# Optimization experiments

Hardware: AMD Instinct MI355X
Metric: run time of the kernel (lower is better)

Reference implementation:

```python
import jax, jax.numpy as jnp
import numpy as np

B, S, IN_DIM = 16, 1024, 64
D, H, FF, L, OUT = 512, 8, 2048, 6, 256
HD = D // H
EPS = 1e-5


def _ln(x, g, b):
    m = jnp.mean(x, axis=-1, keepdims=True)
    v = jnp.var(x, axis=-1, keepdims=True)
    return (x - m) * jax.lax.rsqrt(v + EPS) * g + b


def setup_inputs() -> dict:
    key = jax.random.key(0)
    ks = jax.random.split(key, 24)
    def rn(k, shape, scale=0.02):
        return jax.random.normal(k, shape, dtype=jnp.float32) * scale
    return {
        "x": jax.random.normal(ks[0], (B, S, IN_DIM), dtype=jnp.float32),
        "in_w": rn(ks[1], (IN_DIM, D)), "in_b": jnp.zeros((D,), jnp.float32),
        "in_ln_g": jnp.ones((D,), jnp.float32), "in_ln_b": jnp.zeros((D,), jnp.float32),
        "pos": rn(ks[2], (S, D)),
        "qkv_w": rn(ks[3], (L, D, 3 * D)), "qkv_b": jnp.zeros((L, 3 * D), jnp.float32),
        "ao_w": rn(ks[4], (L, D, D)), "ao_b": jnp.zeros((L, D), jnp.float32),
        "ff_w1": rn(ks[5], (L, D, FF)), "ff_b1": jnp.zeros((L, FF), jnp.float32),
        "ff_w2": rn(ks[6], (L, FF, D)), "ff_b2": jnp.zeros((L, D), jnp.float32),
        "ln1_g": jnp.ones((L, D), jnp.float32), "ln1_b": jnp.zeros((L, D), jnp.float32),
        "ln2_g": jnp.ones((L, D), jnp.float32), "ln2_b": jnp.zeros((L, D), jnp.float32),
        "o_w1": rn(ks[7], (D, D // 2)), "o_b1": jnp.zeros((D // 2,), jnp.float32),
        "o_ln_g": jnp.ones((D // 2,), jnp.float32), "o_ln_b": jnp.zeros((D // 2,), jnp.float32),
        "o_w2": rn(ks[8], (D // 2, OUT)), "o_b2": jnp.zeros((OUT,), jnp.float32),
    }


def reference(x, in_w, in_b, in_ln_g, in_ln_b, pos,
              qkv_w, qkv_b, ao_w, ao_b, ff_w1, ff_b1, ff_w2, ff_b2,
              ln1_g, ln1_b, ln2_g, ln2_b,
              o_w1, o_b1, o_ln_g, o_ln_b, o_w2, o_b2):
    h = x @ in_w + in_b                      # [B,S,D]
    h = _ln(h, in_ln_g, in_ln_b)
    h = h + pos[None, :, :]
    scale = 1.0 / jnp.sqrt(jnp.float32(HD))
    for l in range(L):
        qkv = h @ qkv_w[l] + qkv_b[l]        # [B,S,3D]
        q, k, v = jnp.split(qkv, 3, axis=-1)
        q = q.reshape(B, S, H, HD)
        k = k.reshape(B, S, H, HD)
        v = v.reshape(B, S, H, HD)
        scores = jnp.einsum('bqhd,bkhd->bhqk', q, k) * scale
        attn = jax.nn.softmax(scores, axis=-1)
        ctx = jnp.einsum('bhqk,bkhd->bqhd', attn, v).reshape(B, S, D)
        attn_out = ctx @ ao_w[l] + ao_b[l]
        h = _ln(h + attn_out, ln1_g[l], ln1_b[l])
        ff = jax.nn.gelu(h @ ff_w1[l] + ff_b1[l], approximate=False) @ ff_w2[l] + ff_b2[l]
        h = _ln(h + ff, ln2_g[l], ln2_b[l])
    pooled = jnp.mean(h, axis=1)             # [B,D]
    z = jax.nn.gelu(pooled @ o_w1 + o_b1, approximate=False)
    z = _ln(z, o_ln_g, o_ln_b)
    return z @ o_w2 + o_b2                   # [B,OUT]
```

## Files before the change

### kernel.cpp

```cpp
#include <hip/hip_runtime.h>
#include <hip/hip_bf16.h>

#define B_ 16
#define S_ 1024
#define IN_ 64
#define D_ 512
#define H_ 8
#define HD_ 64
#define FF_ 2048
#define L_ 6
#define OUT_ 256
#define BS_ (B_*S_)

typedef __attribute__((ext_vector_type(8))) short s16x8;
typedef __attribute__((ext_vector_type(4))) short s16x4;
typedef __attribute__((ext_vector_type(4))) float f32x4;

#define AS1(p) ((const __attribute__((address_space(1))) void*)(p))
#define AS3(p) ((__attribute__((address_space(3))) void*)(p))

__device__ __forceinline__ ushort f2bf(float x) {
  __hip_bfloat16 h = __float2bfloat16(x);
  return *reinterpret_cast<ushort*>(&h);
}
__device__ __forceinline__ float bf2f(ushort u) {
  unsigned v = ((unsigned)u) << 16;
  union { unsigned u; float f; } c; c.u = v; return c.f;
}
__device__ __forceinline__ float gelu_exact(float x) {
  return 0.5f * x * (1.0f + erff(x * 0.70710678118654752f));
}

template<int BN, int WM, int WN, int MODE>
__global__ __launch_bounds__(256)
void gemm_bt(const ushort* __restrict__ A, int lda,
             const ushort* __restrict__ Bt, int ldb,
             const float* __restrict__ bias,
             ushort* __restrict__ C, int ldc,
             int K)
{
  constexpr int BM = 128;
  constexpr int BK = 64;
  constexpr int FM = BM / (WM * 16);
  constexpr int FN = BN / (WN * 16);
  __shared__ ushort As[BM * BK];
  __shared__ ushort Bs[BN * BK];

  const int tid = threadIdx.x;
  const int lane = tid & 63;
  const int wave = tid >> 6;
  const int wr = wave / WN;
  const int wc = wave % WN;
  const int lrow = lane & 15;
  const int lk = (lane >> 4) * 8;

  const int gx = gridDim.x;
  const int nwg = gx * gridDim.y;
  const int flat = blockIdx.y * gx + blockIdx.x;
  const int T = (flat & 7) * (nwg >> 3) + (flat >> 3);
  const int m0 = (T / gx) * BM;
  const int n0 = (T % gx) * BN;

  f32x4 acc[FM][FN];
#pragma unroll
  for (int m = 0; m < FM; ++m)
#pragma unroll
    for (int n = 0; n < FN; ++n)
      acc[m][n] = (f32x4){0.f, 0.f, 0.f, 0.f};

  for (int k0 = 0; k0 < K; k0 += BK) {
    __syncthreads();
#pragma unroll
    for (int rr = 0; rr < BM / 32; ++rr) {
      int c = rr * 256 + tid;
      int row = c >> 3, cg = c & 7;
      __builtin_amdgcn_global_load_lds(
          AS1(A + (size_t)(m0 + row) * lda + k0 + cg * 8),
          AS3(As + (size_t)(rr * 256 + wave * 64) * 8), 16, 0, 0);
    }
#pragma unroll
    for (int rr = 0; rr < BN / 32; ++rr) {
      int c = rr * 256 + tid;
      int row = c >> 3, cg = c & 7;
      __builtin_amdgcn_global_load_lds(
          AS1(Bt + (size_t)(n0 + row) * ldb + k0 + cg * 8),
          AS3(Bs + (size_t)(rr * 256 + wave * 64) * 8), 16, 0, 0);
    }
    __syncthreads();
#pragma unroll
    for (int kk = 0; kk < 2; ++kk) {
      s16x8 a[FM], b[FN];
#pragma unroll
      for (int m = 0; m < FM; ++m)
        a[m] = *(const s16x8*)&As[(wr * FM * 16 + m * 16 + lrow) * BK + kk * 32 + lk];
#pragma unroll
      for (int n = 0; n < FN; ++n)
        b[n] = *(const s16x8*)&Bs[(wc * FN * 16 + n * 16 + lrow) * BK + kk * 32 + lk];
#pragma unroll
      for (int m = 0; m < FM; ++m)
#pragma unroll
        for (int n = 0; n < FN; ++n)
          acc[m][n] = __builtin_amdgcn_mfma_f32_16x16x32_bf16(a[m], b[n], acc[m][n], 0, 0, 0);
    }
  }

  const int rb = m0 + wr * FM * 16 + (lane >> 4) * 4;
  const int cb = n0 + wc * FN * 16 + lrow;
#pragma unroll
  for (int n = 0; n < FN; ++n) {
    int col = cb + n * 16;
    float bv = bias ? bias[col] : 0.0f;
#pragma unroll
    for (int m = 0; m < FM; ++m) {
      int row = rb + m * 16;
#pragma unroll
      for (int r = 0; r < 4; ++r) {
        float v = acc[m][n][r] + bv;
        size_t idx = (size_t)(row + r) * ldc + col;
        if (MODE == 1) C[idx] = f2bf(v);
        else           C[idx] = f2bf(gelu_exact(v));
      }
    }
  }
}

__global__ __launch_bounds__(512)
void flash_kernel(const ushort* __restrict__ qkv, const ushort* __restrict__ vt,
                  ushort* __restrict__ ctx)
{
  constexpr int KB = 128;
  const float KE = 0.125f * 1.44269504f;
  __shared__ ushort ks[KB][72];
  __shared__ ushort vs[HD_][KB + 8];
  const int tid = threadIdx.x;
  const int lane = tid & 63;
  const int wave = tid >> 6;
  const int lrow = lane & 15;
  const int g = lane >> 4;
  const int lk = g * 8;

  const int flat = blockIdx.y * 8 + blockIdx.x;
  const int T = (flat & 7) * 128 + (flat >> 3);
  const int bh = T >> 3;
  const int b = bh >> 3, h = bh & 7;
  const int q0 = (T & 7) * 128;

  s16x8 qf[2];
  {
    const ushort* qrow = qkv + ((size_t)(b * S_ + q0 + wave * 16 + lrow)) * (3 * D_) + h * HD_;
    s16x8 r0 = *(const s16x8*)(qrow + lk);
    s16x8 r1 = *(const s16x8*)(qrow + 32 + lk);
#pragma unroll
    for (int j = 0; j < 8; ++j) {
      qf[0][j] = (short)f2bf(bf2f((ushort)r0[j]) * KE);
      qf[1][j] = (short)f2bf(bf2f((ushort)r1[j]) * KE);
    }
  }
  float lsum = 0.f;
  f32x4 o[4] = {};

  for (int kt = 0; kt < S_ / KB; ++kt) {
    __syncthreads();
    for (int c = tid; c < KB * 8; c += 512) {
      int row = c >> 3, cg = c & 7;
      *(s16x8*)&ks[row][cg * 8] =
          *(const s16x8*)(qkv + ((size_t)(b * S_ + kt * KB + row)) * (3 * D_) + D_ + h * HD_ + cg * 8);
    }
    for (int c = tid; c < HD_ * 16; c += 512) {
      int row = c >> 4, cg = c & 15;
      *(s16x8*)&vs[row][cg * 8] =
          *(const s16x8*)(vt + ((size_t)(bh * HD_ + row)) * S_ + kt * KB + cg * 8);
    }
    __syncthreads();

#pragma unroll
    for (int tp = 0; tp < 4; ++tp) {
      f32x4 s0 = {}, s1 = {};
      {
        s16x8 k00 = *(const s16x8*)&ks[tp * 32 + lrow][lk];
        s16x8 k01 = *(const s16x8*)&ks[tp * 32 + lrow][32 + lk];
        s16x8 k10 = *(const s16x8*)&ks[tp * 32 + 16 + lrow][lk];
        s16x8 k11 = *(const s16x8*)&ks[tp * 32 + 16 + lrow][32 + lk];
        s0 = __builtin_amdgcn_mfma_f32_16x16x32_bf16(k00, qf[0], s0, 0, 0, 0);
        s0 = __builtin_amdgcn_mfma_f32_16x16x32_bf16(k01, qf[1], s0, 0, 0, 0);
        s1 = __builtin_amdgcn_mfma_f32_16x16x32_bf16(k10, qf[0], s1, 0, 0, 0);
        s1 = __builtin_amdgcn_mfma_f32_16x16x32_bf16(k11, qf[1], s1, 0, 0, 0);
      }
      union { s16x8 v; unsigned u[4]; } pa;
      {
        float p0 = exp2f(s0[0]), p1 = exp2f(s0[1]);
        float p2 = exp2f(s0[2]), p3 = exp2f(s0[3]);
        float p4 = exp2f(s1[0]), p5 = exp2f(s1[1]);
        float p6 = exp2f(s1[2]), p7 = exp2f(s1[3]);
        lsum += ((p0 + p1) + (p2 + p3)) + ((p4 + p5) + (p6 + p7));
        unsigned u0 = __float_as_uint(p0) + 0x8000u, u1 = __float_as_uint(p1) + 0x8000u;
        unsigned u2 = __float_as_uint(p2) + 0x8000u, u3 = __float_as_uint(p3) + 0x8000u;
        unsigned u4 = __float_as_uint(p4) + 0x8000u, u5 = __float_as_uint(p5) + 0x8000u;
        unsigned u6 = __float_as_uint(p6) + 0x8000u, u7 = __float_as_uint(p7) + 0x8000u;
        pa.u[0] = (u0 >> 16) | (u1 & 0xffff0000u);
        pa.u[1] = (u2 >> 16) | (u3 & 0xffff0000u);
        pa.u[2] = (u4 >> 16) | (u5 & 0xffff0000u);
        pa.u[3] = (u6 >> 16) | (u7 & 0xffff0000u);
      }
#pragma unroll
      for (int n2 = 0; n2 < 4; ++n2) {
        s16x8 vf = *(const s16x8*)&vs[n2 * 16 + lrow][tp * 32 + lk];
        o[n2] = __builtin_amdgcn_mfma_f32_16x16x32_bf16(vf, pa.v, o[n2], 0, 0, 0);
      }
    }
  }
  lsum += __shfl_xor(lsum, 16);
  lsum += __shfl_xor(lsum, 32);
  float inv = 1.0f / lsum;

  ushort* crow = ctx + ((size_t)(b * S_ + q0 + wave * 16 + lrow)) * D_ + h * HD_;
#pragma unroll
  for (int n2 = 0; n2 < 4; ++n2) {
    s16x4 w;
#pragma unroll
    for (int r = 0; r < 4; ++r) w[r] = (short)f2bf(o[n2][r] * inv);
    *(s16x4*)(crow + n2 * 16 + g * 4) = w;
  }
}

__global__ __launch_bounds__(256)
void ln512_kernel(const ushort* __restrict__ a, const ushort* __restrict__ res,
                  const float* __restrict__ g, const float* __restrict__ bt,
                  const float* __restrict__ pos,
                  ushort* __restrict__ hout)
{
  const int row = blockIdx.x;
  const int t = threadIdx.x;
  const size_t base = (size_t)row * D_;
  float x0 = bf2f(a[base + t]), x1 = bf2f(a[base + t + 256]);
  if (res) { x0 += bf2f(res[base + t]); x1 += bf2f(res[base + t + 256]); }
  float s = x0 + x1, q = x0 * x0 + x1 * x1;
#pragma unroll
  for (int m = 32; m > 0; m >>= 1) { s += __shfl_xor(s, m); q += __shfl_xor(q, m); }
  __shared__ float red[8];
  if ((t & 63) == 0) { red[(t >> 6) * 2] = s; red[(t >> 6) * 2 + 1] = q; }
  __syncthreads();
  s = red[0] + red[2] + red[4] + red[6];
  q = red[1] + red[3] + red[5] + red[7];
  float mean = s * (1.0f / D_);
  float var = q * (1.0f / D_) - mean * mean;
  float rs = rsqrtf(var + 1e-5f);
  float y0 = (x0 - mean) * rs * g[t] + bt[t];
  float y1 = (x1 - mean) * rs * g[t + 256] + bt[t + 256];
  if (pos) {
    int sp = row & (S_ - 1);
    y0 += pos[(size_t)sp * D_ + t];
    y1 += pos[(size_t)sp * D_ + t + 256];
  }
  hout[base + t] = f2bf(y0);
  hout[base + t + 256] = f2bf(y1);
}

__global__ __launch_bounds__(256)
void vtrans_kernel(const ushort* __restrict__ qkv, ushort* __restrict__ vt)
{
  __shared__ ushort tile[64][72];
  const int bh = blockIdx.x;
  const int b = bh >> 3, h = bh & 7;
  const int k0 = blockIdx.y * 64;
  const int t = threadIdx.x;
  for (int c = t; c < 512; c += 256) {
    int row = c >> 3, dg = c & 7;
    *(s16x8*)&tile[row][dg * 8] =
        *(const s16x8*)(qkv + (size_t)(b * S_ + k0 + row) * (3 * D_) + 2 * D_ + h * HD_ + dg * 8);
  }
  __syncthreads();
  int d = t >> 2, gg = t & 3;
#pragma unroll
  for (int w = 0; w < 2; ++w) {
    ushort out[8];
#pragma unroll
    for (int j = 0; j < 8; ++j) {
      int lkk = w * 32 + (j < 4 ? 4 * gg + j : 16 + 4 * gg + (j - 4));
      out[j] = tile[lkk][d];
    }
    *(s16x8*)&vt[((size_t)bh * HD_ + d) * S_ + k0 + w * 32 + gg * 8] = *(s16x8*)out;
  }
}

__global__ void wtrans_kernel(const float* __restrict__ W, ushort* __restrict__ Wt, int K, int N)
{
  __shared__ float tile[32][33];
  const float* Wl = W + (size_t)blockIdx.z * K * N;
  ushort* Wtl = Wt + (size_t)blockIdx.z * K * N;
  int n0 = blockIdx.x * 32, k0 = blockIdx.y * 32;
  int tx = threadIdx.x, ty = threadIdx.y;
#pragma unroll
  for (int r = 0; r < 4; ++r)
    tile[ty * 4 + r][tx] = Wl[(size_t)(k0 + ty * 4 + r) * N + n0 + tx];
  __syncthreads();
#pragma unroll
  for (int r = 0; r < 4; ++r)
    Wtl[(size_t)(n0 + ty * 4 + r) * K + k0 + tx] = f2bf(tile[tx][ty * 4 + r]);
}

__global__ void castx_kernel(const float* __restrict__ x, ushort* __restrict__ xb, int n)
{
  int i = blockIdx.x * blockDim.x + threadIdx.x;
  if (i < n) xb[i] = f2bf(x[i]);
}

__global__ __launch_bounds__(256)
void pool_partial_kernel(const ushort* __restrict__ h, float* __restrict__ pp)
{
  int b = blockIdx.x, ch = blockIdx.y;
  int t = threadIdx.x;
  float s0 = 0, s1 = 0;
  for (int r = 0; r < 128; ++r) {
    size_t base = ((size_t)b * S_ + ch * 128 + r) * D_;
    s0 += bf2f(h[base + t]);
    s1 += bf2f(h[base + t + 256]);
  }
  pp[(size_t)(b * 8 + ch) * D_ + t] = s0;
  pp[(size_t)(b * 8 + ch) * D_ + t + 256] = s1;
}

__global__ __launch_bounds__(256)
void head_kernel(const float* __restrict__ pp,
                 const float* __restrict__ w1, const float* __restrict__ b1,
                 const float* __restrict__ lg, const float* __restrict__ lb,
                 const float* __restrict__ w2, const float* __restrict__ b2,
                 float* __restrict__ out)
{
  __shared__ float pooled[D_];
  __shared__ float z[256];
  int b = blockIdx.x, t = threadIdx.x;
  for (int i = t; i < D_; i += 256) {
    float s = 0;
    for (int c = 0; c < 8; ++c) s += pp[(size_t)(b * 8 + c) * D_ + i];
    pooled[i] = s * (1.0f / S_);
  }
  __syncthreads();
  float acc = 0;
  for (int k = 0; k < D_; ++k) acc += pooled[k] * w1[(size_t)k * 256 + t];
  float zz = gelu_exact(acc + b1[t]);
  float s = zz, q = zz * zz;
#pragma unroll
  for (int m = 32; m > 0; m >>= 1) { s += __shfl_xor(s, m); q += __shfl_xor(q, m); }
  __shared__ float red[8];
  if ((t & 63) == 0) { red[(t >> 6) * 2] = s; red[(t >> 6) * 2 + 1] = q; }
  __syncthreads();
  s = red[0] + red[2] + red[4] + red[6];
  q = red[1] + red[3] + red[5] + red[7];
  float mean = s * (1.0f / 256), var = q * (1.0f / 256) - mean * mean;
  float rs = rsqrtf(var + 1e-5f);
  z[t] = (zz - mean) * rs * lg[t] + lb[t];
  __syncthreads();
  float o = 0;
  for (int k = 0; k < 256; ++k) o += z[k] * w2[(size_t)k * 256 + t];
  out[(size_t)b * 256 + t] = o + b2[t];
}

extern "C" void kernel_launch(void* const* d_in, const int* in_sizes, int n_in,
                              void* d_out, int out_size, void* d_ws, size_t ws_size,
                              hipStream_t stream)
{
  const float* x       = (const float*)d_in[0];
  const float* in_w    = (const float*)d_in[1];
  const float* in_b    = (const float*)d_in[2];
  const float* in_ln_g = (const float*)d_in[3];
  const float* in_ln_b = (const float*)d_in[4];
  const float* pos     = (const float*)d_in[5];
  const float* qkv_w   = (const float*)d_in[6];
  const float* qkv_b   = (const float*)d_in[7];
  const float* ao_w    = (const float*)d_in[8];
  const float* ao_b    = (const float*)d_in[9];
  const float* ff_w1   = (const float*)d_in[10];
  const float* ff_b1   = (const float*)d_in[11];
  const float* ff_w2   = (const float*)d_in[12];
  const float* ff_b2   = (const float*)d_in[13];
  const float* ln1_g   = (const float*)d_in[14];
  const float* ln1_b   = (const float*)d_in[15];
  const float* ln2_g   = (const float*)d_in[16];
  const float* ln2_b   = (const float*)d_in[17];
  const float* o_w1    = (const float*)d_in[18];
  const float* o_b1    = (const float*)d_in[19];
  const float* o_ln_g  = (const float*)d_in[20];
  const float* o_ln_b  = (const float*)d_in[21];
  const float* o_w2    = (const float*)d_in[22];
  const float* o_b2    = (const float*)d_in[23];

  char* wp = (char*)d_ws;
  auto alloc = [&](size_t bytes) {
    char* p = wp;
    wp += (bytes + 255) & ~(size_t)255;
    return p;
  };
  ushort* hb     = (ushort*)alloc((size_t)BS_ * D_ * 2);
  ushort* tmpb   = (ushort*)alloc((size_t)BS_ * D_ * 2);
  ushort* big    = (ushort*)alloc((size_t)BS_ * FF_ * 2);
  ushort* ctxb   = (ushort*)alloc((size_t)BS_ * D_ * 2);
  ushort* xb     = (ushort*)alloc((size_t)BS_ * IN_ * 2);
  ushort* vt     = (ushort*)alloc((size_t)B_ * H_ * HD_ * S_ * 2);
  float*  pp     = (float*) alloc((size_t)B_ * 8 * D_ * 4);
  ushort* in_wt  = (ushort*)alloc((size_t)D_ * IN_ * 2);
  ushort* qkv_wt = (ushort*)alloc((size_t)L_ * 3 * D_ * D_ * 2);
  ushort* ao_wt  = (ushort*)alloc((size_t)L_ * D_ * D_ * 2);
  ushort* ff1_wt = (ushort*)alloc((size_t)L_ * FF_ * D_ * 2);
  ushort* ff2_wt = (ushort*)alloc((size_t)L_ * D_ * FF_ * 2);
  (void)ws_size; (void)n_in; (void)in_sizes; (void)out_size;

  dim3 wb(32, 8);
  wtrans_kernel<<<dim3(D_ / 32, IN_ / 32, 1), wb, 0, stream>>>(in_w, in_wt, IN_, D_);
  wtrans_kernel<<<dim3(3 * D_ / 32, D_ / 32, L_), wb, 0, stream>>>(qkv_w, qkv_wt, D_, 3 * D_);
  wtrans_kernel<<<dim3(D_ / 32, D_ / 32, L_), wb, 0, stream>>>(ao_w, ao_wt, D_, D_);
  wtrans_kernel<<<dim3(FF_ / 32, D_ / 32, L_), wb, 0, stream>>>(ff_w1, ff1_wt, D_, FF_);
  wtrans_kernel<<<dim3(D_ / 32, FF_ / 32, L_), wb, 0, stream>>>(ff_w2, ff2_wt, FF_, D_);
  castx_kernel<<<BS_ * IN_ / 256, 256, 0, stream>>>(x, xb, BS_ * IN_);

  gemm_bt<128, 2, 2, 1><<<dim3(D_ / 128, BS_ / 128), 256, 0, stream>>>(
      xb, IN_, in_wt, IN_, in_b, tmpb, D_, IN_);
  ln512_kernel<<<BS_, 256, 0, stream>>>(tmpb, nullptr, in_ln_g, in_ln_b, pos, hb);

  for (int l = 0; l < L_; ++l) {
    gemm_bt<128, 2, 2, 1><<<dim3(3 * D_ / 128, BS_ / 128), 256, 0, stream>>>(
        hb, D_, qkv_wt + (size_t)l * 3 * D_ * D_, D_, qkv_b + (size_t)l * 3 * D_,
        big, 3 * D_, D_);
    vtrans_kernel<<<dim3(B_ * H_, S_ / 64), 256, 0, stream>>>(big, vt);
    flash_kernel<<<dim3(S_ / 128, B_ * H_), 512, 0, stream>>>(big, vt, ctxb);
    gemm_bt<128, 2, 2, 1><<<dim3(D_ / 128, BS_ / 128), 256, 0, stream>>>(
        ctxb, D_, ao_wt + (size_t)l * D_ * D_, D_, ao_b + (size_t)l * D_,
        tmpb, D_, D_);
    ln512_kernel<<<BS_, 256, 0, stream>>>(tmpb, hb, ln1_g + (size_t)l * D_,
                                          ln1_b + (size_t)l * D_, nullptr, hb);
    gemm_bt<128, 2, 2, 2><<<dim3(FF_ / 128, BS_ / 128), 256, 0, stream>>>(
        hb, D_, ff1_wt + (size_t)l * FF_ * D_, D_, ff_b1 + (size_t)l * FF_,
        big, FF_, D_);
    gemm_bt<128, 2, 2, 1><<<dim3(D_ / 128, BS_ / 128), 256, 0, stream>>>(
        big, FF_, ff2_wt + (size_t)l * D_ * FF_, FF_, ff_b2 + (size_t)l * D_,
        tmpb, D_, FF_);
    ln512_kernel<<<BS_, 256, 0, stream>>>(tmpb, hb, ln2_g + (size_t)l * D_,
                                          ln2_b + (size_t)l * D_, nullptr, hb);
  }
  pool_partial_kernel<<<dim3(B_, 8), 256, 0, stream>>>(hb, pp);
  head_kernel<<<B_, 256, 0, stream>>>(pp, o_w1, o_b1, o_ln_g, o_ln_b, o_w2, o_b2,
                                      (float*)d_out);
}
```

Before: 1.813 ms.

## Stage GEMM epilogue through LDS and fuse V transpose into QKV GEMM

The GEMM epilogue now writes results into a shared-memory tile that reuses the A/B staging buffers, then emits coalesced 16-byte global stores instead of scattered 2-byte stores. A new MODE 3 writes the V projection straight into the transposed per-head layout the flash kernel expects. The QKV GEMM is split into a Q/K launch and a V launch, which removes the separate vtrans kernel and its extra read and write of V. In exchange there is an extra launch, one more barrier per tile, and LDS bank traffic in the epilogue.

```diff
diff --git a/kernel.cpp b/kernel.cpp
--- a/kernel.cpp
+++ b/kernel.cpp
@@ -43,8 +43,11 @@
   constexpr int BK = 64;
   constexpr int FM = BM / (WM * 16);
   constexpr int FN = BN / (WN * 16);
-  __shared__ ushort As[BM * BK];
-  __shared__ ushort Bs[BN * BK];
+  constexpr int CP = 136;
+  __shared__ union {
+    struct { ushort a[BM * BK]; ushort b[BN * BK]; } s;
+    ushort c[BM * CP];
+  } u;
 
   const int tid = threadIdx.x;
   const int lane = tid & 63;
@@ -76,7 +79,7 @@
       int row = c >> 3, cg = c & 7;
       __builtin_amdgcn_global_load_lds(
           AS1(A + (size_t)(m0 + row) * lda + k0 + cg * 8),
-          AS3(As + (size_t)(rr * 256 + wave * 64) * 8), 16, 0, 0);
+          AS3(u.s.a + (size_t)(rr * 256 + wave * 64) * 8), 16, 0, 0);
     }
 #pragma unroll
     for (int rr = 0; rr < BN / 32; ++rr) {
@@ -84,7 +87,7 @@
       int row = c >> 3, cg = c & 7;
       __builtin_amdgcn_global_load_lds(
           AS1(Bt + (size_t)(n0 + row) * ldb + k0 + cg * 8),
-          AS3(Bs + (size_t)(rr * 256 + wave * 64) * 8), 16, 0, 0);
+          AS3(u.s.b + (size_t)(rr * 256 + wave * 64) * 8), 16, 0, 0);
     }
     __syncthreads();
 #pragma unroll
@@ -92,10 +95,10 @@
       s16x8 a[FM], b[FN];
 #pragma unroll
       for (int m = 0; m < FM; ++m)
-        a[m] = *(const s16x8*)&As[(wr * FM * 16 + m * 16 + lrow) * BK + kk * 32 + lk];
+        a[m] = *(const s16x8*)&u.s.a[(wr * FM * 16 + m * 16 + lrow) * BK + kk * 32 + lk];
 #pragma unroll
       for (int n = 0; n < FN; ++n)
-        b[n] = *(const s16x8*)&Bs[(wc * FN * 16 + n * 16 + lrow) * BK + kk * 32 + lk];
+        b[n] = *(const s16x8*)&u.s.b[(wc * FN * 16 + n * 16 + lrow) * BK + kk * 32 + lk];
 #pragma unroll
       for (int m = 0; m < FM; ++m)
 #pragma unroll
@@ -104,22 +107,49 @@
     }
   }
 
-  const int rb = m0 + wr * FM * 16 + (lane >> 4) * 4;
-  const int cb = n0 + wc * FN * 16 + lrow;
+  __syncthreads();
+  const int rbL = wr * FM * 16 + (lane >> 4) * 4;
+  const int cbL = wc * FN * 16 + lrow;
 #pragma unroll
   for (int n = 0; n < FN; ++n) {
-    int col = cb + n * 16;
-    float bv = bias ? bias[col] : 0.0f;
+    int colL = cbL + n * 16;
+    float bv = bias ? bias[n0 + colL] : 0.0f;
 #pragma unroll
     for (int m = 0; m < FM; ++m) {
-      int row = rb + m * 16;
 #pragma unroll
       for (int r = 0; r < 4; ++r) {
         float v = acc[m][n][r] + bv;
-        size_t idx = (size_t)(row + r) * ldc + col;
-        if (MODE == 1) C[idx] = f2bf(v);
-        else           C[idx] = f2bf(gelu_exact(v));
+        if (MODE == 2) v = gelu_exact(v);
+        u.c[(rbL + m * 16 + r) * CP + colL] = f2bf(v);
       }
+    }
+  }
+  __syncthreads();
+  if (MODE == 3) {
+    int dl = tid >> 1, kh = tid & 1;
+    int vcol = n0 + dl;
+    int bb = m0 >> 10, k0r = m0 & 1023;
+    ushort* vrow = C + ((size_t)(bb * 8 + (vcol >> 6)) * HD_ + (vcol & 63)) * S_
+                   + k0r + kh * 64;
+#pragma unroll
+    for (int w2 = 0; w2 < 2; ++w2)
+#pragma unroll
+      for (int g2 = 0; g2 < 4; ++g2) {
+        ushort outv[8];
+#pragma unroll
+        for (int jj = 0; jj < 8; ++jj) {
+          int pk = kh * 64 + w2 * 32 + (jj < 4 ? 4 * g2 + jj : 16 + 4 * g2 + (jj - 4));
+          outv[jj] = u.c[pk * CP + dl];
+        }
+        *(s16x8*)(vrow + w2 * 32 + g2 * 8) = *(s16x8*)outv;
+      }
+  } else {
+#pragma unroll
+    for (int p = 0; p < 8; ++p) {
+      int row = p * 16 + (tid >> 4);
+      int col = (tid & 15) * 8;
+      s16x8 v = *(const s16x8*)&u.c[row * CP + col];
+      *(s16x8*)&C[(size_t)(m0 + row) * ldc + n0 + col] = v;
     }
   }
 }
@@ -256,33 +286,6 @@
   hout[base + t + 256] = f2bf(y1);
 }
 
-__global__ __launch_bounds__(256)
-void vtrans_kernel(const ushort* __restrict__ qkv, ushort* __restrict__ vt)
-{
-  __shared__ ushort tile[64][72];
-  const int bh = blockIdx.x;
-  const int b = bh >> 3, h = bh & 7;
-  const int k0 = blockIdx.y * 64;
-  const int t = threadIdx.x;
-  for (int c = t; c < 512; c += 256) {
-    int row = c >> 3, dg = c & 7;
-    *(s16x8*)&tile[row][dg * 8] =
-        *(const s16x8*)(qkv + (size_t)(b * S_ + k0 + row) * (3 * D_) + 2 * D_ + h * HD_ + dg * 8);
-  }
-  __syncthreads();
-  int d = t >> 2, gg = t & 3;
-#pragma unroll
-  for (int w = 0; w < 2; ++w) {
-    ushort out[8];
-#pragma unroll
-    for (int j = 0; j < 8; ++j) {
-      int lkk = w * 32 + (j < 4 ? 4 * gg + j : 16 + 4 * gg + (j - 4));
-      out[j] = tile[lkk][d];
-    }
-    *(s16x8*)&vt[((size_t)bh * HD_ + d) * S_ + k0 + w * 32 + gg * 8] = *(s16x8*)out;
-  }
-}
-
 __global__ void wtrans_kernel(const float* __restrict__ W, ushort* __restrict__ Wt, int K, int N)
 {
   __shared__ float tile[32][33];
@@ -418,10 +421,12 @@
   ln512_kernel<<<BS_, 256, 0, stream>>>(tmpb, nullptr, in_ln_g, in_ln_b, pos, hb);
 
   for (int l = 0; l < L_; ++l) {
-    gemm_bt<128, 2, 2, 1><<<dim3(3 * D_ / 128, BS_ / 128), 256, 0, stream>>>(
-        hb, D_, qkv_wt + (size_t)l * 3 * D_ * D_, D_, qkv_b + (size_t)l * 3 * D_,
-        big, 3 * D_, D_);
-    vtrans_kernel<<<dim3(B_ * H_, S_ / 64), 256, 0, stream>>>(big, vt);
+    const ushort* qwt = qkv_wt + (size_t)l * 3 * D_ * D_;
+    const float*  qb  = qkv_b + (size_t)l * 3 * D_;
+    gemm_bt<128, 2, 2, 1><<<dim3(2 * D_ / 128, BS_ / 128), 256, 0, stream>>>(
+        hb, D_, qwt, D_, qb, big, 3 * D_, D_);
+    gemm_bt<128, 2, 2, 3><<<dim3(D_ / 128, BS_ / 128), 256, 0, stream>>>(
+        hb, D_, qwt + (size_t)(2 * D_) * D_, D_, qb + 2 * D_, vt, S_, D_);
     flash_kernel<<<dim3(S_ / 128, B_ * H_), 512, 0, stream>>>(big, vt, ctxb);
     gemm_bt<128, 2, 2, 1><<<dim3(D_ / 128, BS_ / 128), 256, 0, stream>>>(
         ctxb, D_, ao_wt + (size_t)l * D_ * D_, D_, ao_b + (size_t)l * D_,
```

After: 1.830 ms. About the same (+1.0%).
